# Optimization experiments

Measured on AMD Instinct MI355X. Metric: run time of the kernel, lower is better.

## Reference

```python
import jax, jax.numpy as jnp
import numpy as np

B, W, N = 64, 128, 64
EGC, EGL = 8, 12          # Graph_Constructor dim, GraphLearning embed dim
HID = 77                  # ceil(0.6 * window_size)
ET = 2 * N                # gatv2 doubles embed_dim (= n_features by default)
TOPK = 20
SLOPE = 0.2               # leaky relu alpha


def _batch_edges(e, batch, n):
    # replicate (2,E) edge list per batch element with node offset i*n
    off = (jnp.arange(batch, dtype=e.dtype) * n)[None, :, None]
    return (e[:, None, :] + off).reshape(2, -1)


def setup_inputs() -> dict:
    key = jax.random.key(0)
    ks = jax.random.split(key, 20)
    g = lambda i, shp, s=0.1: jax.random.normal(ks[i], shp, jnp.float32) * s
    p = {
        "x": jax.random.normal(ks[0], (B, W, N), jnp.float32),
        # Graph_Constructor (only used to build edges in preprocessing)
        "emb1": g(1, (N, EGC), 1.0), "emb2": g(2, (N, EGC), 1.0),
        "gc_w1": g(3, (EGC, EGC)), "gc_b1": jnp.zeros(EGC, jnp.float32),
        "gc_w2": g(4, (EGC, EGC)), "gc_b2": jnp.zeros(EGC, jnp.float32),
        # GraphLearning
        "gl_embed": g(5, (N, EGL), 1.0),
        "gcn_w": g(6, (W + EGL, W)), "gcn_b": jnp.zeros(W, jnp.float32),
        "mlp_w1": g(7, (W, HID)), "mlp_b1": jnp.zeros(HID, jnp.float32),
        "mlp_w2": g(8, (HID, W)), "mlp_b2": jnp.zeros(W, jnp.float32),
        # TemporalAttentionLayer (use_gatv2=True): lin: 2N -> ET, a: (ET,1)
        "ta_w": g(9, (2 * N, ET)), "ta_b": jnp.zeros(ET, jnp.float32),
        "ta_a": g(10, (ET,), 1.0), "ta_bias": jnp.zeros((W, W), jnp.float32),
        # GATConv(window, window)
        "gat_w": g(11, (W, W)), "gat_asrc": g(12, (W,), 1.0),
        "gat_adst": g(13, (W,), 1.0), "gat_b": jnp.zeros(W, jnp.float32),
        # forecasting head Linear(W,1)
        "fc_w": g(14, (W, 1)), "fc_b": jnp.zeros(1, jnp.float32),
    }
    # ---- Graph_Constructor edge preprocessing (top-20 neighbors/node) ----
    n1 = jnp.tanh(3.0 * (p["emb1"] @ p["gc_w1"] + p["gc_b1"]))
    n2 = jnp.tanh(3.0 * (p["emb2"] @ p["gc_w2"] + p["gc_b2"]))
    a = n1 @ n2.T - n2 @ n1.T
    adj = jax.nn.relu(jnp.tanh(3.0 * a))
    noise = jax.random.uniform(ks[15], (N, N), jnp.float32) * 0.01
    _, t1 = jax.lax.top_k(adj + noise, TOPK)            # (N, 20)
    rows = jnp.repeat(jnp.arange(N), TOPK)
    edges = jnp.stack([rows, t1.reshape(-1)]).astype(jnp.int32)
    # ---- GraphLearning cosine-similarity edges (keep N^2 - ceil(0.6 N^2)) ----
    wgt = p["gl_embed"]
    nrm = jnp.linalg.norm(wgt, axis=-1)
    cos = (wgt @ wgt.T) / (nrm[:, None] * nrm[None, :])
    n_keep = N * N - int(np.ceil(0.6 * N * N))          # 1638
    _, idx = jax.lax.top_k(cos.reshape(-1), n_keep)
    idx = jnp.sort(idx)                                  # coo row-major order
    gl_edges = jnp.stack([idx // N, idx % N]).astype(jnp.int32)
    p["batch_edge_index"] = _batch_edges(edges, B, N)        # (2, 20*N*B)
    p["gl_batch_edge_index"] = _batch_edges(gl_edges, B, N)  # (2, 1638*B)
    return p


def _gcn(x, ei, w, b, nseg):
    # GCNConv: self-loops + symmetric degree normalization
    src, dst = ei[0], ei[1]
    sl = jnp.arange(nseg, dtype=ei.dtype)
    src = jnp.concatenate([src, sl]); dst = jnp.concatenate([dst, sl])
    deg = jax.ops.segment_sum(jnp.ones(dst.shape, jnp.float32), dst, nseg)
    dinv = jax.lax.rsqrt(jnp.maximum(deg, 1.0))
    h = x @ w
    msg = h[src] * (dinv[src] * dinv[dst])[:, None]
    return jax.ops.segment_sum(msg, dst, nseg) + b


def _gat(x, ei, w, asrc, adst, b, nseg):
    # single-head GATConv with self-loops, softmax over incoming edges
    src, dst = ei[0], ei[1]
    sl = jnp.arange(nseg, dtype=ei.dtype)
    src = jnp.concatenate([src, sl]); dst = jnp.concatenate([dst, sl])
    h = x @ w
    e = jax.nn.leaky_relu(h[src] @ asrc + h[dst] @ adst, SLOPE)
    emax = jax.ops.segment_max(e, dst, nseg)
    ee = jnp.exp(e - emax[dst])
    denom = jax.ops.segment_sum(ee, dst, nseg)
    alpha = ee / denom[dst]
    return jax.ops.segment_sum(h[src] * alpha[:, None], dst, nseg) + b


def _temporal_attn(v, w, bl, a, bias):
    # GATv2-style: e[b,i,j] = a . leakyrelu(W [v_i || v_j] + bl) + bias[i,j]
    # split W to avoid materializing the (B,K,K,2N) concat tensor
    wi, wj = w[:N], w[N:]
    left = v @ wi            # (B,K,ET)
    right = v @ wj           # (B,K,ET)
    s = jax.nn.leaky_relu(left[:, :, None, :] + right[:, None, :, :] + bl, SLOPE)
    e = jnp.einsum('bije,e->bij', s, a) + bias          # (B,K,K)
    attn = jax.nn.softmax(e, axis=2)                    # dropout off (eval)
    return jnp.tanh(attn @ v)                           # (B,K,N)


def reference(x, emb1, emb2, gc_w1, gc_b1, gc_w2, gc_b2, gl_embed, gcn_w, gcn_b,
              mlp_w1, mlp_b1, mlp_w2, mlp_b2, ta_w, ta_b, ta_a, ta_bias,
              gat_w, gat_asrc, gat_adst, gat_b, fc_w, fc_b,
              batch_edge_index, gl_batch_edge_index):
    Bn = B * N
    xp = jnp.transpose(x, (0, 2, 1))                    # (B,N,W)
    x_batch = xp.reshape(Bn, W)
    # ---- GraphLearning: concat node embeddings, GCN, relu, tanh MLP ----
    all_emb = jnp.tile(gl_embed, (B, 1))                # (B*N, 12)
    h = _gcn(jnp.concatenate([x_batch, all_emb], 1), gl_batch_edge_index,
             gcn_w, gcn_b, Bn)
    h = jax.nn.relu(h)
    x_rec = jnp.tanh(jnp.tanh(h @ mlp_w1 + mlp_b1) @ mlp_w2 + mlp_b2)  # (B*N,W)
    # ---- residual + temporal attention over window dim ----
    xs = x_batch + x_rec
    v = jnp.transpose(xs.reshape(B, N, W), (0, 2, 1))   # (B,W,N)
    ht = _temporal_attn(v, ta_w, ta_b, ta_a, ta_bias)   # (B,W,N)
    # ---- feature GAT + forecasting head ----
    hg = jnp.transpose(ht, (0, 2, 1)).reshape(Bn, W)
    hg = _gat(hg, batch_edge_index, gat_w, gat_asrc, gat_adst, gat_b, Bn)
    x_pre = jnp.tanh(hg @ fc_w + fc_b).reshape(B, 1, N)
    out_rec = jnp.transpose(x_rec.reshape(B, N, W), (0, 2, 1))  # (B,W,N)
    return out_rec, x_pre
```

## Files before the change

kernel.cpp:

```cpp
#include <hip/hip_runtime.h>
#include <math.h>

#define BB  64
#define WW  128
#define NN  64
#define HIDN 77

__global__ __launch_bounds__(512) void k_front(
    const float* __restrict__ x, const float* __restrict__ emb,
    const float* __restrict__ wg, const float* __restrict__ gcn_b,
    const float* __restrict__ w1, const float* __restrict__ b1,
    const float* __restrict__ w2, const float* __restrict__ b2,
    const int* __restrict__ gl_ei, int E_gl,
    const int* __restrict__ gat_ei, int E_gat,
    const float* __restrict__ gat_w, const float* __restrict__ asrc,
    const float* __restrict__ adst, const float* __restrict__ fcw,
    const float* __restrict__ gat_b,
    float* __restrict__ xs, float* __restrict__ out_rec,
    float* __restrict__ VAV, int* __restrict__ gat_off, int* __restrict__ gat_list) {
  __shared__ float smem[20448];
  float* Ws   = smem;
  float* XA   = smem + 17920;
  float* Sm   = smem + 19072;
  float* hm   = smem + 19616;
  float* gbb  = smem + 20256;
  int*   cnt  = (int*)(smem + 20384);
  float* recT = smem + 17920;

  int tid = threadIdx.x;

  if (blockIdx.x >= 512) {
    int which = blockIdx.x - 512;
    if (which < 3) {
      const float* vecg = (which == 0) ? asrc : (which == 1) ? adst : fcw;
      if (tid < 128) {
        float acc = 0.f;
#pragma unroll 4
        for (int k = 0; k < 128; k++) acc += gat_w[tid * 128 + k] * vecg[k];
        VAV[which * 128 + tid] = acc;
      }
      if (which == 2) {
        float* red = smem;
        if (tid < 128) red[tid] = gat_b[tid] * fcw[tid];
        __syncthreads();
        if (tid == 0) {
          float s = 0.f;
          for (int i = 0; i < 128; i++) s += red[i];
          VAV[384] = s;
        }
      }
    } else {
      int* ip   = (int*)smem;
      int* offs = ip;
      int* cur  = ip + 65;
      int* cntg = ip + 129;
      int* lst  = ip + 193;
      if (tid < 64) cntg[tid] = 1;
      __syncthreads();
      for (int e = tid; e < E_gat; e += 512) atomicAdd(&cntg[gat_ei[BB * E_gat + e]], 1);
      __syncthreads();
      if (tid == 0) { int s = 0; for (int n = 0; n < 64; n++) { offs[n] = s; s += cntg[n]; } offs[64] = s; }
      __syncthreads();
      if (tid < 64) cur[tid] = offs[tid];
      __syncthreads();
      for (int e = tid; e < E_gat; e += 512) {
        int src = gat_ei[e], dst = gat_ei[BB * E_gat + e];
        lst[atomicAdd(&cur[dst], 1)] = src;
      }
      if (tid < 64) lst[atomicAdd(&cur[tid], 1)] = tid;
      __syncthreads();
      if (tid < 65) gat_off[tid] = offs[tid];
      int tot = offs[64];
      for (int t = tid; t < tot; t += 512) gat_list[t] = lst[t];
    }
    return;
  }

  int r0 = blockIdx.x * 8;
  int b = r0 >> 6, n0 = r0 & 63;
  const float* xb = x + (size_t)b * 8192;

  {
    const float4* W4 = (const float4*)wg;
    float4* Ws4 = (float4*)Ws;
    for (int t = tid; t < 4480; t += 512) Ws4[t] = W4[t];
  }
  for (int t = tid; t < 544; t += 512) Sm[t] = 0.f;
  if (tid < 128) gbb[tid] = gcn_b[tid];
  if (tid < 64) cnt[tid] = 1;
  __syncthreads();

  for (int e = tid; e < E_gl; e += 512) {
    int dst = gl_ei[BB * E_gl + e];
    atomicAdd(&cnt[dst], 1);
    int d = dst - n0;
    if ((unsigned)d < 8u) Sm[d * 68 + gl_ei[e]] = 1.0f;
  }
  __syncthreads();

  for (int t = tid; t < 544; t += 512) {
    int i = t / 68, s = t % 68;
    if (s < 64) {
      float di = rsqrtf((float)cnt[n0 + i]);
      float v = Sm[t] * rsqrtf((float)cnt[s]) * di;
      if (s == n0 + i) v += di * di;
      Sm[t] = v;
    }
  }
  __syncthreads();

  {
    int i = tid >> 6, tw = tid & 63;
    const float* Sr = Sm + i * 68;
    float o0 = 0, o1 = 0;
#pragma unroll 4
    for (int s4 = 0; s4 < 16; s4++) {
      float4 sv = *(const float4*)&Sr[s4 * 4];
      float4 x0 = *(const float4*)&xb[tw * 64 + s4 * 4];
      float4 x1 = *(const float4*)&xb[(tw + 64) * 64 + s4 * 4];
      o0 += sv.x * x0.x + sv.y * x0.y + sv.z * x0.z + sv.w * x0.w;
      o1 += sv.x * x1.x + sv.y * x1.y + sv.z * x1.z + sv.w * x1.w;
    }
    float* Xr = XA + i * 144;
    Xr[tw] = o0; Xr[tw + 64] = o1;
  }
  if (tid < 96) {
    int i = tid / 12, j = tid % 12;
    const float* Sr = Sm + i * 68;
    float a = 0.f;
    for (int s = 0; s < 64; s++) a += Sr[s] * emb[s * 12 + j];
    XA[i * 144 + 128 + j] = a;
  }
  __syncthreads();

  {
    int row = tid >> 6, cg = tid & 63;
    int c0 = cg * 2;
    float a0 = 0, a1 = 0;
    const float* Ar = XA + row * 144;
#pragma unroll 4
    for (int k = 0; k < 140; k++) {
      float2 wv = *(const float2*)&Ws[k * 128 + c0];
      float a = Ar[k];
      a0 += a * wv.x; a1 += a * wv.y;
    }
    __syncthreads();
    float2 bv = *(const float2*)&gbb[c0];
    XA[row * 144 + c0]     = fmaxf(a0 + bv.x, 0.f);
    XA[row * 144 + c0 + 1] = fmaxf(a1 + bv.y, 0.f);
    for (int q = tid; q < 10240; q += 512) {
      int k = q / 80, c = q % 80;
      Ws[q] = (c < HIDN) ? w1[k * HIDN + c] : 0.f;
    }
  }
  __syncthreads();

  {
    bool act = tid < 320;
    if (act) {
      int rp = tid / 40, cg = tid % 40;
      int c0 = cg * 2;
      float a0 = 0, a1 = 0;
      const float* Ar = XA + rp * 144;
#pragma unroll 4
      for (int k = 0; k < 128; k++) {
        float2 wv = *(const float2*)&Ws[k * 80 + c0];
        float a = Ar[k];
        a0 += a * wv.x; a1 += a * wv.y;
      }
      float b0 = (c0 < HIDN) ? b1[c0] : 0.f;
      float b1v = (c0 + 1 < HIDN) ? b1[c0 + 1] : 0.f;
      hm[rp * 80 + c0]     = tanhf(a0 + b0);
      hm[rp * 80 + c0 + 1] = tanhf(a1 + b1v);
    }
  }
  __syncthreads();
  {
    const float4* w24 = (const float4*)w2;
    float4* Wb4 = (float4*)smem;
    for (int t = tid; t < 2464; t += 512) Wb4[t] = w24[t];
  }
  __syncthreads();

  {
    int row = tid >> 6, cg = tid & 63;
    int c0 = cg * 2;
    float a0 = 0, a1 = 0;
    const float* Hr = hm + row * 80;
#pragma unroll 4
    for (int k = 0; k < HIDN; k++) {
      float2 wv = *(const float2*)&smem[k * 128 + c0];
      float a = Hr[k];
      a0 += a * wv.x; a1 += a * wv.y;
    }
    float x0 = tanhf(a0 + b2[c0]);
    float x1 = tanhf(a1 + b2[c0 + 1]);
    int nn = n0 + row;
    float s0 = x0 + xb[c0 * 64 + nn];
    float s1 = x1 + xb[(c0 + 1) * 64 + nn];
    *(float2*)&xs[(size_t)(r0 + row) * 128 + c0] = make_float2(s0, s1);
    recT[c0 * 9 + row] = x0;
    recT[(c0 + 1) * 9 + row] = x1;
  }
  __syncthreads();
  float* orc = out_rec + (size_t)b * 8192 + n0;
  for (int t = tid; t < 1024; t += 512) {
    int w = t >> 3, i = t & 7;
    orc[w * 64 + i] = recT[w * 9 + i];
  }
}

__global__ __launch_bounds__(512) void k_attn(const float* __restrict__ xs, const float* __restrict__ ta_w,
                                              const float* __restrict__ ta_b, const float* __restrict__ ta_a,
                                              const float* __restrict__ ta_bias, const float* __restrict__ VAV,
                                              float* __restrict__ PART) {
  __shared__ float smem[38272];
  float* Rf  = smem;
  float* XN  = smem + 16384;
  float* WT  = smem + 25088;
  float* Lh  = smem + 33408;
  float* av2 = smem + 37632;
  float* av6 = smem + 37760;
  float* tbs = smem + 37888;
  float* uu  = smem + 38016;
  float* vv  = smem + 38048;
  float* vva = smem + 38176;
  float* vvd = smem + 38208;
  float* vvf = smem + 38240;
  float* scratch = WT;

  int tid = threadIdx.x;
  int b = blockIdx.x >> 2, q = blockIdx.x & 3;
  int i0 = q * 32;

  {
    const float* xsb = xs + (size_t)b * 8192;
#pragma unroll
    for (int t = 0; t < 16; t++) {
      int idx = tid + t * 512;
      XN[(idx >> 7) * 136 + (idx & 127)] = xsb[idx];
    }
  }
#pragma unroll
  for (int t = 0; t < 16; t++) {
    int idx = tid + t * 512;
    int e = idx & 127, n = idx >> 7;
    WT[e * 65 + n] = ta_w[(64 + n) * 128 + e];
  }
  if (tid < 128) {
    float a = ta_a[tid];
    av2[tid] = 0.4f * a; av6[tid] = 0.6f * a;
    tbs[tid] = ta_b[tid];
  }
  if (tid >= 128 && tid < 160) {
    int i = tid - 128;
    vva[i] = VAV[i0 + i];
    vvd[i] = VAV[128 + i0 + i];
    vvf[i] = VAV[256 + i0 + i];
  }
  __syncthreads();

  {
    int et = tid >> 4, jt = tid & 15;
    int e0 = et * 4, j0 = jt * 8;
    float acc[4][8];
#pragma unroll
    for (int r = 0; r < 4; r++)
#pragma unroll
      for (int c = 0; c < 8; c++) acc[r][c] = 0.f;
#pragma unroll 4
    for (int n = 0; n < 64; n++) {
      float4 b0 = *(const float4*)&XN[n * 136 + j0];
      float4 b1 = *(const float4*)&XN[n * 136 + j0 + 4];
      float bb[8] = {b0.x, b0.y, b0.z, b0.w, b1.x, b1.y, b1.z, b1.w};
#pragma unroll
      for (int r = 0; r < 4; r++) {
        float a = WT[(e0 + r) * 65 + n];
#pragma unroll
        for (int c = 0; c < 8; c++) acc[r][c] += a * bb[c];
      }
    }
#pragma unroll
    for (int r = 0; r < 4; r++) {
      *(float4*)&Rf[(e0 + r) * 128 + j0] = make_float4(acc[r][0], acc[r][1], acc[r][2], acc[r][3]);
      *(float4*)&Rf[(e0 + r) * 128 + j0 + 4] = make_float4(acc[r][4], acc[r][5], acc[r][6], acc[r][7]);
    }
  }
  __syncthreads();
#pragma unroll
  for (int t = 0; t < 16; t++) {
    int idx = tid + t * 512;
    int e = idx & 127, n = idx >> 7;
    WT[e * 65 + n] = ta_w[n * 128 + e];
  }
  __syncthreads();

  {
    int e = tid >> 2, ig = tid & 3;
    int ii = ig * 8;
    float acc[8];
#pragma unroll
    for (int c = 0; c < 8; c++) acc[c] = 0.f;
#pragma unroll 4
    for (int n = 0; n < 64; n++) {
      float4 b0 = *(const float4*)&XN[n * 136 + i0 + ii];
      float4 b1 = *(const float4*)&XN[n * 136 + i0 + ii + 4];
      float a = WT[e * 65 + n];
      acc[0] += a * b0.x; acc[1] += a * b0.y; acc[2] += a * b0.z; acc[3] += a * b0.w;
      acc[4] += a * b1.x; acc[5] += a * b1.y; acc[6] += a * b1.z; acc[7] += a * b1.w;
    }
    float tb = tbs[e];
#pragma unroll
    for (int c = 0; c < 8; c++) Lh[e * 32 + ii + c] = acc[c] + tb;
  }
  __syncthreads();

  if (tid < 160) {
    float acc = 0.f;
    if (tid < 128) {
      for (int e = 0; e < 128; e++) acc += av6[e] * Rf[e * 128 + tid];
      vv[tid] = acc;
    } else {
      int i = tid - 128;
      for (int e = 0; e < 128; e++) acc += av6[e] * Lh[e * 32 + i];
      uu[i] = acc;
    }
  }
  __syncthreads();

  bool act = tid < 256;
  int tj = tid & 31, ti = (tid >> 5) & 7;
  float p[4][4];
  if (act) {
    float acc[4][4];
#pragma unroll
    for (int a = 0; a < 4; a++)
#pragma unroll
      for (int j = 0; j < 4; j++) acc[a][j] = 0.f;
#pragma unroll 2
    for (int e = 0; e < 128; e++) {
      float4 Lv = *(const float4*)&Lh[e * 32 + ti * 4];
      float4 Rv = *(const float4*)&Rf[e * 128 + tj * 4];
      float ae = av2[e];
      float La[4] = {Lv.x, Lv.y, Lv.z, Lv.w};
      float Ra[4] = {Rv.x, Rv.y, Rv.z, Rv.w};
#pragma unroll
      for (int a = 0; a < 4; a++)
#pragma unroll
        for (int j = 0; j < 4; j++) {
          float t = La[a] + Ra[j];
          acc[a][j] += ae * fabsf(t);
        }
    }
#pragma unroll
    for (int a = 0; a < 4; a++) {
      int i = i0 + ti * 4 + a;
      float uvi = uu[ti * 4 + a];
      float4 bv = *(const float4*)&ta_bias[(size_t)i * 128 + tj * 4];
      float v0 = acc[a][0] + bv.x + uvi + vv[tj * 4 + 0];
      float v1 = acc[a][1] + bv.y + uvi + vv[tj * 4 + 1];
      float v2 = acc[a][2] + bv.z + uvi + vv[tj * 4 + 2];
      float v3 = acc[a][3] + bv.w + uvi + vv[tj * 4 + 3];
      float m = fmaxf(fmaxf(v0, v1), fmaxf(v2, v3));
#pragma unroll
      for (int o = 16; o > 0; o >>= 1) m = fmaxf(m, __shfl_xor(m, o));
      float e0 = __expf(v0 - m), e1 = __expf(v1 - m), e2 = __expf(v2 - m), e3 = __expf(v3 - m);
      float s = e0 + e1 + e2 + e3;
#pragma unroll
      for (int o = 16; o > 0; o >>= 1) s += __shfl_xor(s, o);
      float inv = 1.f / s;
      p[a][0] = e0 * inv; p[a][1] = e1 * inv; p[a][2] = e2 * inv; p[a][3] = e3 * inv;
    }
  }
  __syncthreads();
  float* P = Lh;
  if (act) {
#pragma unroll
    for (int a = 0; a < 4; a++)
      *(float4*)&P[(ti * 4 + a) * 132 + tj * 4] = make_float4(p[a][0], p[a][1], p[a][2], p[a][3]);
  }
  __syncthreads();

  int tn = tid & 15, i2 = tid >> 4;
  float o0 = 0, o1 = 0, o2 = 0, o3 = 0;
  const float* Prow = P + i2 * 132;
  const float* X0 = XN + (tn +  0) * 136;
  const float* X1 = XN + (tn + 16) * 136;
  const float* X2 = XN + (tn + 32) * 136;
  const float* X3 = XN + (tn + 48) * 136;
#pragma unroll 4
  for (int j4 = 0; j4 < 32; j4++) {
    float4 pv = *(const float4*)&Prow[j4 * 4];
    float4 a0 = *(const float4*)&X0[j4 * 4];
    float4 a1 = *(const float4*)&X1[j4 * 4];
    float4 a2 = *(const float4*)&X2[j4 * 4];
    float4 a3 = *(const float4*)&X3[j4 * 4];
    o0 += pv.x * a0.x + pv.y * a0.y + pv.z * a0.z + pv.w * a0.w;
    o1 += pv.x * a1.x + pv.y * a1.y + pv.z * a1.z + pv.w * a1.w;
    o2 += pv.x * a2.x + pv.y * a2.y + pv.z * a2.z + pv.w * a2.w;
    o3 += pv.x * a3.x + pv.y * a3.y + pv.z * a3.z + pv.w * a3.w;
  }
  float t0 = tanhf(o0), t1 = tanhf(o1), t2 = tanhf(o2), t3 = tanhf(o3);
  {
    float wa = vva[i2], wd = vvd[i2], wf = vvf[i2];
    int base = i2 * 66 + tn;
    scratch[base +  0] = t0 * wa; scratch[base + 16] = t1 * wa;
    scratch[base + 32] = t2 * wa; scratch[base + 48] = t3 * wa;
    scratch[2112 + base +  0] = t0 * wd; scratch[2112 + base + 16] = t1 * wd;
    scratch[2112 + base + 32] = t2 * wd; scratch[2112 + base + 48] = t3 * wd;
    scratch[4224 + base +  0] = t0 * wf; scratch[4224 + base + 16] = t1 * wf;
    scratch[4224 + base + 32] = t2 * wf; scratch[4224 + base + 48] = t3 * wf;
  }
  __syncthreads();
  if (tid < 192) {
    int arr = tid >> 6, n = tid & 63;
    const float* sp = scratch + arr * 2112 + n;
    float s = 0.f;
#pragma unroll 8
    for (int i = 0; i < 32; i++) s += sp[i * 66];
    PART[(size_t)b * 768 + q * 192 + arr * 64 + n] = s;
  }
}

__global__ __launch_bounds__(64) void k_fin(const float* __restrict__ PART, const float* __restrict__ VAV,
                                            const int* __restrict__ off, const int* __restrict__ list,
                                            const float* __restrict__ fcb, float* __restrict__ outp) {
  __shared__ float ss_s[64], sd_s[64], pf_s[64];
  int tid = threadIdx.x, b = blockIdx.x;
  const float* pb = PART + (size_t)b * 768;
  {
    float s0 = 0, s1 = 0, s2 = 0;
#pragma unroll
    for (int q2 = 0; q2 < 4; q2++) {
      const float* p = pb + q2 * 192;
      s0 += p[tid]; s1 += p[64 + tid]; s2 += p[128 + tid];
    }
    ss_s[tid] = s0; sd_s[tid] = s1; pf_s[tid] = s2;
  }
  __syncthreads();
  int e0 = off[tid], e1 = off[tid + 1];
  float sdv = sd_s[tid];
  float mx = -1e30f;
  for (int e = e0; e < e1; e++) {
    float t = ss_s[list[e]] + sdv;
    t = fmaxf(t, 0.2f * t);
    mx = fmaxf(mx, t);
  }
  float den = 0.f, acc = 0.f;
  for (int e = e0; e < e1; e++) {
    int s = list[e];
    float t = ss_s[s] + sdv;
    t = fmaxf(t, 0.2f * t);
    float w = __expf(t - mx);
    den += w;
    acc += w * pf_s[s];
  }
  outp[b * 64 + tid] = tanhf(acc / den + VAV[384] + fcb[0]);
}

extern "C" void kernel_launch(void* const* d_in, const int* in_sizes, int n_in,
                              void* d_out, int out_size, void* d_ws, size_t ws_size,
                              hipStream_t stream) {
  (void)n_in; (void)out_size; (void)ws_size;
  const float* x        = (const float*)d_in[0];
  const float* gl_embed = (const float*)d_in[7];
  const float* gcn_w    = (const float*)d_in[8];
  const float* gcn_b    = (const float*)d_in[9];
  const float* mlp_w1   = (const float*)d_in[10];
  const float* mlp_b1   = (const float*)d_in[11];
  const float* mlp_w2   = (const float*)d_in[12];
  const float* mlp_b2   = (const float*)d_in[13];
  const float* ta_w     = (const float*)d_in[14];
  const float* ta_b     = (const float*)d_in[15];
  const float* ta_a     = (const float*)d_in[16];
  const float* ta_bias  = (const float*)d_in[17];
  const float* gat_w    = (const float*)d_in[18];
  const float* gat_asrc = (const float*)d_in[19];
  const float* gat_adst = (const float*)d_in[20];
  const float* gat_b    = (const float*)d_in[21];
  const float* fc_w     = (const float*)d_in[22];
  const float* fc_b     = (const float*)d_in[23];
  const int*   gat_ei   = (const int*)d_in[24];
  const int*   gl_ei    = (const int*)d_in[25];

  int E_gat = in_sizes[24] / (2 * BB);
  int E_gl  = in_sizes[25] / (2 * BB);

  float* ws = (float*)d_ws;
  float* XS    = ws + 0;
  int*   IP    = (int*)(ws + 524288);
  int* GATOFF  = IP;
  int* GATLIST = IP + 72;
  float* VAV   = ws + 526848;
  float* PART  = ws + 527360;

  float* out_rec = (float*)d_out;
  float* out_pre = (float*)d_out + 524288;

  k_front<<<516, 512, 0, stream>>>(x, gl_embed, gcn_w, gcn_b, mlp_w1, mlp_b1, mlp_w2, mlp_b2,
                                   gl_ei, E_gl, gat_ei, E_gat,
                                   gat_w, gat_asrc, gat_adst, fc_w, gat_b,
                                   XS, out_rec, VAV, GATOFF, GATLIST);
  k_attn<<<256, 512, 0, stream>>>(XS, ta_w, ta_b, ta_a, ta_bias, VAV, PART);
  k_fin<<<64, 64, 0, stream>>>(PART, VAV, GATOFF, GATLIST, fc_b, out_pre);
}
```

Baseline: 80.56 us.

## Shrink shared-memory footprint and stage input tile transposed in LDS

Shared memory drops from 20448 to 19696 floats by reusing regions. The GCN bias now comes from global memory, the hidden buffer sits over the dead adjacency area, and the MLP weight padding shrinks from 80 to 78 columns. The GCN weight load is split into two phases so its first half can share space with a new transposed copy of the input tile. The aggregation then reads that copy from LDS instead of doing strided global float4 loads. The likely aim is to fit two blocks per CU. The cost is an extra barrier and a large staging copy, and the hidden buffer now overlaps the degree counters.

```diff
diff --git a/kernel.cpp b/kernel.cpp
--- a/kernel.cpp
+++ b/kernel.cpp
@@ -18,14 +18,14 @@
     const float* __restrict__ gat_b,
     float* __restrict__ xs, float* __restrict__ out_rec,
     float* __restrict__ VAV, int* __restrict__ gat_off, int* __restrict__ gat_list) {
-  __shared__ float smem[20448];
+  __shared__ float smem[19696];
   float* Ws   = smem;
+  float* XT   = smem + 9600;
   float* XA   = smem + 17920;
+  float* recT = smem + 17920;
   float* Sm   = smem + 19072;
-  float* hm   = smem + 19616;
-  float* gbb  = smem + 20256;
-  int*   cnt  = (int*)(smem + 20384);
-  float* recT = smem + 17920;
+  int*   cnt  = (int*)(smem + 19616);
+  float* hm   = smem + 19072;
 
   int tid = threadIdx.x;
 
@@ -83,10 +83,11 @@
   {
     const float4* W4 = (const float4*)wg;
     float4* Ws4 = (float4*)Ws;
-    for (int t = tid; t < 4480; t += 512) Ws4[t] = W4[t];
-  }
+    for (int t = tid; t < 2400; t += 512) Ws4[t] = W4[t];
+  }
+  for (int t = tid; t < 8192; t += 512)
+    XT[(t & 63) * 129 + (t >> 6)] = xb[t];
   for (int t = tid; t < 544; t += 512) Sm[t] = 0.f;
-  if (tid < 128) gbb[tid] = gcn_b[tid];
   if (tid < 64) cnt[tid] = 1;
   __syncthreads();
 
@@ -114,15 +115,13 @@
     const float* Sr = Sm + i * 68;
     float o0 = 0, o1 = 0;
 #pragma unroll 4
-    for (int s4 = 0; s4 < 16; s4++) {
-      float4 sv = *(const float4*)&Sr[s4 * 4];
-      float4 x0 = *(const float4*)&xb[tw * 64 + s4 * 4];
-      float4 x1 = *(const float4*)&xb[(tw + 64) * 64 + s4 * 4];
-      o0 += sv.x * x0.x + sv.y * x0.y + sv.z * x0.z + sv.w * x0.w;
-      o1 += sv.x * x1.x + sv.y * x1.y + sv.z * x1.z + sv.w * x1.w;
-    }
-    float* Xr = XA + i * 144;
-    Xr[tw] = o0; Xr[tw + 64] = o1;
+    for (int s = 0; s < 64; s++) {
+      float sv = Sr[s];
+      o0 += sv * XT[s * 129 + tw];
+      o1 += sv * XT[s * 129 + tw + 64];
+    }
+    XA[i * 144 + tw] = o0;
+    XA[i * 144 + tw + 64] = o1;
   }
   if (tid < 96) {
     int i = tid / 12, j = tid % 12;
@@ -134,6 +133,13 @@
   __syncthreads();
 
   {
+    const float4* W4 = (const float4*)wg;
+    float4* Ws4 = (float4*)Ws;
+    for (int t = tid; t < 2080; t += 512) Ws4[2400 + t] = W4[2400 + t];
+  }
+  __syncthreads();
+
+  {
     int row = tid >> 6, cg = tid & 63;
     int c0 = cg * 2;
     float a0 = 0, a1 = 0;
@@ -145,33 +151,31 @@
       a0 += a * wv.x; a1 += a * wv.y;
     }
     __syncthreads();
-    float2 bv = *(const float2*)&gbb[c0];
-    XA[row * 144 + c0]     = fmaxf(a0 + bv.x, 0.f);
-    XA[row * 144 + c0 + 1] = fmaxf(a1 + bv.y, 0.f);
-    for (int q = tid; q < 10240; q += 512) {
-      int k = q / 80, c = q % 80;
+    XA[row * 144 + c0]     = fmaxf(a0 + gcn_b[c0], 0.f);
+    XA[row * 144 + c0 + 1] = fmaxf(a1 + gcn_b[c0 + 1], 0.f);
+    for (int q = tid; q < 9984; q += 512) {
+      int k = q / 78, c = q % 78;
       Ws[q] = (c < HIDN) ? w1[k * HIDN + c] : 0.f;
     }
   }
   __syncthreads();
 
   {
-    bool act = tid < 320;
-    if (act) {
-      int rp = tid / 40, cg = tid % 40;
+    if (tid < 312) {
+      int rp = tid / 39, cg = tid % 39;
       int c0 = cg * 2;
       float a0 = 0, a1 = 0;
       const float* Ar = XA + rp * 144;
 #pragma unroll 4
       for (int k = 0; k < 128; k++) {
-        float2 wv = *(const float2*)&Ws[k * 80 + c0];
+        float2 wv = *(const float2*)&Ws[k * 78 + c0];
         float a = Ar[k];
         a0 += a * wv.x; a1 += a * wv.y;
       }
-      float b0 = (c0 < HIDN) ? b1[c0] : 0.f;
+      float b0v = (c0 < HIDN) ? b1[c0] : 0.f;
       float b1v = (c0 + 1 < HIDN) ? b1[c0 + 1] : 0.f;
-      hm[rp * 80 + c0]     = tanhf(a0 + b0);
-      hm[rp * 80 + c0 + 1] = tanhf(a1 + b1v);
+      hm[rp * 78 + c0]     = tanhf(a0 + b0v);
+      hm[rp * 78 + c0 + 1] = tanhf(a1 + b1v);
     }
   }
   __syncthreads();
@@ -186,7 +190,7 @@
     int row = tid >> 6, cg = tid & 63;
     int c0 = cg * 2;
     float a0 = 0, a1 = 0;
-    const float* Hr = hm + row * 80;
+    const float* Hr = hm + row * 78;
 #pragma unroll 4
     for (int k = 0; k < HIDN; k++) {
       float2 wv = *(const float2*)&smem[k * 128 + c0];
```

Result: faster. 73.01 us (-9.4%).
